# Kernel tuning notes

Measured on AMD Instinct MI355X. Metric: run time of the kernel, lower is better.

Reference implementation:

```python
import jax, jax.numpy as jnp
import numpy as np

D_MODEL = 1024
N_HEADS = 16
D_HEAD = D_MODEL // N_HEADS
D_FF = 4 * D_MODEL
B, T = 2, 2048
LN_EPS = 1e-5


def layer_norm(x, g, b):
    mu = jnp.mean(x, axis=-1, keepdims=True)
    var = jnp.mean(jnp.square(x - mu), axis=-1, keepdims=True)
    return (x - mu) * jax.lax.rsqrt(var + LN_EPS) * g + b


def setup_inputs() -> dict:
    key = jax.random.key(0)
    ks = jax.random.split(key, 8)
    s = lambda fan: 1.0 / np.sqrt(fan)
    return {
        "x": jax.random.normal(ks[0], (B, T, D_MODEL), dtype=jnp.float32),
        "ln1_g": jnp.ones((D_MODEL,), jnp.float32),
        "ln1_b": jnp.zeros((D_MODEL,), jnp.float32),
        "Wqkv": jax.random.normal(ks[1], (D_MODEL, 3 * D_MODEL), jnp.float32) * s(D_MODEL),
        "Wout": jax.random.normal(ks[2], (D_MODEL, D_MODEL), jnp.float32) * s(D_MODEL),
        "ln2_g": jnp.ones((D_MODEL,), jnp.float32),
        "ln2_b": jnp.zeros((D_MODEL,), jnp.float32),
        "W1": jax.random.normal(ks[3], (D_MODEL, D_FF), jnp.float32) * s(D_MODEL),
        "b1": jnp.zeros((D_FF,), jnp.float32),
        "W2": jax.random.normal(ks[4], (D_FF, D_MODEL), jnp.float32) * s(D_FF),
        "b2": jnp.zeros((D_MODEL,), jnp.float32),
    }


def attention(x, Wqkv, Wout):
    Bx, Tx, C = x.shape
    qkv = x @ Wqkv  # [B,T,3C]
    q, k, v = jnp.split(qkv, 3, axis=-1)
    q = q.reshape(Bx, Tx, N_HEADS, D_HEAD)
    k = k.reshape(Bx, Tx, N_HEADS, D_HEAD)
    v = v.reshape(Bx, Tx, N_HEADS, D_HEAD)
    scores = jnp.einsum('bqhd,bkhd->bhqk', q, k) / np.sqrt(D_HEAD).astype(np.float32)
    causal = jnp.tril(jnp.ones((Tx, Tx), dtype=bool))
    scores = jnp.where(causal, scores, -jnp.inf)
    attn = jax.nn.softmax(scores, axis=-1)
    out = jnp.einsum('bhqk,bkhd->bqhd', attn, v).reshape(Bx, Tx, C)
    return out @ Wout


def reference(x, ln1_g, ln1_b, Wqkv, Wout, ln2_g, ln2_b, W1, b1, W2, b2):
    x = x + attention(layer_norm(x, ln1_g, ln1_b), Wqkv, Wout)
    h = layer_norm(x, ln2_g, ln2_b)
    h = jax.nn.gelu(h @ W1 + b1, approximate=False) @ W2 + b2
    return x + h
```

## Files before the change

### kernel.cpp

```cpp
#include <hip/hip_runtime.h>
#include <math.h>

typedef __bf16 bf16;
typedef __bf16 bf16x4 __attribute__((ext_vector_type(4)));
typedef __bf16 bf16x8 __attribute__((ext_vector_type(8)));
typedef float  f32x4  __attribute__((ext_vector_type(4)));

#define MFMA16(a,b,c) __builtin_amdgcn_mfma_f32_16x16x32_bf16((a),(b),(c),0,0,0)

static __device__ __forceinline__ bf16x8 combine8(const bf16* plo, const bf16* phi) {
  bf16x4 lo = *(const bf16x4*)plo;
  bf16x4 hi = *(const bf16x4*)phi;
  return __builtin_shufflevector(lo, hi, 0, 1, 2, 3, 4, 5, 6, 7);
}

__global__ __launch_bounds__(256) void transpose_cast(const float* __restrict__ W,
                                                      bf16* __restrict__ WT,
                                                      int K, int N) {
  __shared__ float t[32][33];
  int n0 = blockIdx.x * 32, k0 = blockIdx.y * 32;
  int tx = threadIdx.x, ty = threadIdx.y;
#pragma unroll
  for (int i = 0; i < 32; i += 8)
    t[ty + i][tx] = W[(size_t)(k0 + ty + i) * N + n0 + tx];
  __syncthreads();
#pragma unroll
  for (int i = 0; i < 32; i += 8)
    WT[(size_t)(n0 + ty + i) * K + k0 + tx] = (bf16)t[tx][ty + i];
}

__global__ __launch_bounds__(256) void ln_kernel(const float* __restrict__ X,
                                                 const float* __restrict__ g,
                                                 const float* __restrict__ bta,
                                                 bf16* __restrict__ out) {
  int row  = blockIdx.x * 4 + (threadIdx.x >> 6);
  int lane = threadIdx.x & 63;
  const float4* x4 = (const float4*)(X + (size_t)row * 1024);
  float4 v[4];
  float s = 0.f, ss = 0.f;
#pragma unroll
  for (int i = 0; i < 4; ++i) {
    v[i] = x4[i * 64 + lane];
    s  += v[i].x + v[i].y + v[i].z + v[i].w;
    ss += v[i].x * v[i].x + v[i].y * v[i].y + v[i].z * v[i].z + v[i].w * v[i].w;
  }
#pragma unroll
  for (int off = 1; off < 64; off <<= 1) {
    s  += __shfl_xor(s, off, 64);
    ss += __shfl_xor(ss, off, 64);
  }
  float mu  = s * (1.0f / 1024.0f);
  float var = ss * (1.0f / 1024.0f) - mu * mu;
  float rs  = rsqrtf(var + 1e-5f);
  bf16* orow = out + (size_t)row * 1024;
#pragma unroll
  for (int i = 0; i < 4; ++i) {
    int c = i * 256 + lane * 4;
    bf16x4 pk;
    pk[0] = (bf16)((v[i].x - mu) * rs * g[c + 0] + bta[c + 0]);
    pk[1] = (bf16)((v[i].y - mu) * rs * g[c + 1] + bta[c + 1]);
    pk[2] = (bf16)((v[i].z - mu) * rs * g[c + 2] + bta[c + 2]);
    pk[3] = (bf16)((v[i].w - mu) * rs * g[c + 3] + bta[c + 3]);
    *(bf16x4*)(orow + c) = pk;
  }
}

template <int NR>
static __device__ __forceinline__ void stage2(const bf16* const* srcs, int koff,
                                              unsigned char* lds_base, int wv) {
#pragma unroll
  for (int i = 0; i < NR; ++i)
    __builtin_amdgcn_global_load_lds(
        (const __attribute__((address_space(1))) void*)(srcs[i] + koff),
        (__attribute__((address_space(3))) void*)(lds_base + (wv * (NR * 8) + i * 8) * 128),
        16, 0, 0);
}

static __device__ __forceinline__ bf16x8 frag_ld(const unsigned char* lds_base,
                                                 int r, int u) {
  return *(const bf16x8*)(lds_base + r * 128 + (((u ^ (r & 7)) & 7) << 4));
}

static __device__ __forceinline__ float gelu_tanh(float v) {
  float t = 0.7978845608028654f * (v + 0.044715f * v * v * v);
  t = fminf(t, 15.0f);
  float e = __builtin_amdgcn_exp2f(2.8853900817779268f * t);
  float th = (e - 1.0f) * __builtin_amdgcn_rcpf(e + 1.0f);
  return 0.5f * v * (1.0f + th);
}

template <int EPI, int BM>
__global__ __launch_bounds__(256) void gemm_bt(const bf16* __restrict__ A,
                                               const bf16* __restrict__ BT,
                                               int K, int N, int gx,
                                               const float* __restrict__ bias,
                                               const float* __restrict__ res,
                                               bf16* __restrict__ outb,
                                               float* __restrict__ outf) {
  constexpr int MI = BM / 32;
  constexpr int ANR = BM / 32;
  constexpr int TILE = (BM + 128) * 128;
  __shared__ unsigned char smem[TILE * 2];
  int nwg = gridDim.x, bid = blockIdx.x;
  int nb = (bid & 7) * (nwg >> 3) + (bid >> 3);
  int bx = nb % gx, by = nb / gx;
  int brow = by * BM, bcol = bx * 128;
  int tid = threadIdx.x, wv = tid >> 6, lane = tid & 63;
  int l15 = lane & 15, l4 = lane >> 4;
  int wm = wv >> 1, wn = wv & 1;
  f32x4 acc[MI][4] = {};

  int sr = lane >> 3;
  int su = (lane & 7) ^ sr;
  const bf16* aptr[ANR];
#pragma unroll
  for (int i = 0; i < ANR; ++i)
    aptr[i] = A + (size_t)(brow + wv * (ANR * 8) + i * 8 + sr) * K + su * 8;
  const bf16* bptr[4];
#pragma unroll
  for (int i = 0; i < 4; ++i)
    bptr[i] = BT + (size_t)(bcol + wv * 32 + i * 8 + sr) * K + su * 8;

  stage2<ANR>(aptr, 0, smem, wv);
  stage2<4>(bptr, 0, smem + BM * 128, wv);
  __syncthreads();
  int cur = 0;
  for (int k0 = 0; k0 < K; k0 += 64) {
    unsigned char* sc = smem + cur * TILE;
    if (k0 + 64 < K) {
      unsigned char* sn = smem + (cur ^ 1) * TILE;
      stage2<ANR>(aptr, k0 + 64, sn, wv);
      stage2<4>(bptr, k0 + 64, sn + BM * 128, wv);
    }
    unsigned char* As = sc;
    unsigned char* Bs = sc + BM * 128;
#pragma unroll
    for (int ks = 0; ks < 2; ++ks) {
      bf16x8 af[MI], bfr[4];
#pragma unroll
      for (int mi = 0; mi < MI; ++mi)
        af[mi] = frag_ld(As, wm * (BM / 2) + mi * 16 + l15, ks * 4 + l4);
#pragma unroll
      for (int ni = 0; ni < 4; ++ni)
        bfr[ni] = frag_ld(Bs, wn * 64 + ni * 16 + l15, ks * 4 + l4);
#pragma unroll
      for (int mi = 0; mi < MI; ++mi)
#pragma unroll
        for (int ni = 0; ni < 4; ++ni)
          acc[mi][ni] = MFMA16(af[mi], bfr[ni], acc[mi][ni]);
    }
    __syncthreads();
    cur ^= 1;
  }
#pragma unroll
  for (int mi = 0; mi < MI; ++mi) {
#pragma unroll
    for (int ni = 0; ni < 4; ++ni) {
      int col  = bcol + wn * 64 + ni * 16 + l15;
      int row0 = brow + wm * (BM / 2) + mi * 16 + l4 * 4;
#pragma unroll
      for (int r = 0; r < 4; ++r) {
        int row = row0 + r;
        float v = acc[mi][ni][r];
        if (EPI == 1) {
          v += bias[col];
          v = gelu_tanh(v);
        }
        if (EPI == 2) v += res[(size_t)row * N + col];
        if (EPI == 3) v += bias[col] + res[(size_t)row * N + col];
        if (EPI == 0 || EPI == 1) outb[(size_t)row * N + col] = (bf16)v;
        else                      outf[(size_t)row * N + col] = v;
      }
    }
  }
}

__global__ __launch_bounds__(256) void pack_kv(const bf16* __restrict__ qkv,
                                               bf16* __restrict__ kpack,
                                               bf16* __restrict__ vpack) {
  int blk = blockIdx.x;
  int wv = threadIdx.x >> 6, lane = threadIdx.x & 63;
  int l15 = lane & 15, l4 = lane >> 4;
  int ch = (blk & 15) * 4 + wv;
  int bh = blk >> 4;
  int b = bh >> 4, h = bh & 15;
  const bf16* kq = qkv + (size_t)b * 2048 * 3072 + 1024 + h * 64;
  const bf16* vq = kq + 1024;
#pragma unroll
  for (int fr = 0; fr < 4; ++fr) {
    int key = ch * 32 + ((fr >> 1) << 4) + l15;
    int dbase = ((fr & 1) << 5) + l4 * 4;
    bf16x8 v = combine8(kq + (size_t)key * 3072 + dbase,
                        kq + (size_t)key * 3072 + dbase + 16);
    *(bf16x8*)(kpack + ((size_t)(bh * 64 + ch) * 4 + fr) * 512 + lane * 8) = v;
  }
#pragma unroll
  for (int db = 0; db < 4; ++db) {
    int d = db * 16 + l15;
    bf16x8 v;
#pragma unroll
    for (int j = 0; j < 8; ++j) {
      int key = ch * 32 + l4 * 4 + (j & 3) + ((j >> 2) << 4);
      v[j] = vq[(size_t)key * 3072 + d];
    }
    *(bf16x8*)(vpack + ((size_t)(bh * 64 + ch) * 4 + db) * 512 + lane * 8) = v;
  }
}

static __device__ __forceinline__ void proc_chunk(
    const bf16x8* __restrict__ kf, const bf16x8* __restrict__ vf,
    const bf16x8 (* __restrict__ qf)[2], f32x4 (* __restrict__ o)[4],
    float* __restrict__ lsum, bool diag, int l15, int l4) {
  const float SC = 0.125f * 1.4426950408889634f;
#pragma unroll
  for (int f = 0; f < 2; ++f) {
    f32x4 c0 = {0.f, 0.f, 0.f, 0.f}, c1 = {0.f, 0.f, 0.f, 0.f};
    c0 = MFMA16(kf[0], qf[f][0], c0);
    c0 = MFMA16(kf[1], qf[f][1], c0);
    c1 = MFMA16(kf[2], qf[f][0], c1);
    c1 = MFMA16(kf[3], qf[f][1], c1);
    bf16x8 pf;
    float ls = 0.f;
#pragma unroll
    for (int r = 0; r < 4; ++r) {
      float e0 = __builtin_amdgcn_exp2f(c0[r] * SC);
      float e1 = __builtin_amdgcn_exp2f(c1[r] * SC);
      if (diag) {
        int qg = f * 16 + l15;
        int key = l4 * 4 + r;
        if (key > qg)      e0 = 0.f;
        if (key + 16 > qg) e1 = 0.f;
      }
      ls += e0 + e1;
      pf[r]     = (bf16)e0;
      pf[4 + r] = (bf16)e1;
    }
    lsum[f] += ls;
    o[f][0] = MFMA16(vf[0], pf, o[f][0]);
    o[f][1] = MFMA16(vf[1], pf, o[f][1]);
    o[f][2] = MFMA16(vf[2], pf, o[f][2]);
    o[f][3] = MFMA16(vf[3], pf, o[f][3]);
  }
}

__global__ __launch_bounds__(256) void attn_kernel(const bf16* __restrict__ qkv,
                                                   const bf16* __restrict__ kpack,
                                                   const bf16* __restrict__ vpack,
                                                   bf16* __restrict__ attn_out) {
  __shared__ float mbuf[3 * 68 * 64];
  int bid = blockIdx.x;
  int nb = (bid & 7) * 128 + (bid >> 3);
  int bh = nb >> 5, j = nb & 31;
  int b = bh >> 4, h = bh & 15;
  int wv = threadIdx.x >> 6, lane = threadIdx.x & 63;
  int l15 = lane & 15, l4 = lane >> 4;
  int qc[2] = {j, 63 - j};
  const bf16* base = qkv + (size_t)b * 2048 * 3072;
  int d0 = l4 * 4;
  bf16x8 qf[2][2][2];
#pragma unroll
  for (int c = 0; c < 2; ++c)
#pragma unroll
    for (int f = 0; f < 2; ++f) {
      const bf16* qp = base + (size_t)(qc[c] * 32 + f * 16 + l15) * 3072 + h * 64;
      qf[c][f][0] = combine8(qp + d0,      qp + d0 + 16);
      qf[c][f][1] = combine8(qp + d0 + 32, qp + d0 + 48);
    }
  const bf16* kp0 = kpack + (size_t)bh * 64 * 2048 + lane * 8;
  const bf16* vp0 = vpack + (size_t)bh * 64 * 2048 + lane * 8;

  f32x4 o[2][2][4] = {};
  float lsum[2][2] = {};

  for (int ch = wv; ch <= qc[1]; ch += 4) {
    const bf16* kp = kp0 + (size_t)ch * 2048;
    const bf16* vp = vp0 + (size_t)ch * 2048;
    bf16x8 kf[4], vf[4];
    kf[0] = *(const bf16x8*)(kp);
    kf[1] = *(const bf16x8*)(kp + 512);
    kf[2] = *(const bf16x8*)(kp + 1024);
    kf[3] = *(const bf16x8*)(kp + 1536);
    vf[0] = *(const bf16x8*)(vp);
    vf[1] = *(const bf16x8*)(vp + 512);
    vf[2] = *(const bf16x8*)(vp + 1024);
    vf[3] = *(const bf16x8*)(vp + 1536);
    if (ch <= qc[0])
      proc_chunk(kf, vf, qf[0], o[0], lsum[0], ch == qc[0], l15, l4);
    proc_chunk(kf, vf, qf[1], o[1], lsum[1], ch == qc[1], l15, l4);
  }

  if (wv > 0) {
    float* dst = mbuf + (wv - 1) * 68 * 64 + lane;
#pragma unroll
    for (int c = 0; c < 2; ++c)
#pragma unroll
      for (int f = 0; f < 2; ++f) {
#pragma unroll
        for (int db = 0; db < 4; ++db)
#pragma unroll
          for (int r = 0; r < 4; ++r)
            dst[(c * 32 + f * 16 + db * 4 + r) * 64] = o[c][f][db][r];
        dst[(64 + c * 2 + f) * 64] = lsum[c][f];
      }
  }
  __syncthreads();
  if (wv == 0) {
#pragma unroll
    for (int w = 0; w < 3; ++w) {
      const float* src = mbuf + w * 68 * 64 + lane;
#pragma unroll
      for (int c = 0; c < 2; ++c)
#pragma unroll
        for (int f = 0; f < 2; ++f) {
#pragma unroll
          for (int db = 0; db < 4; ++db)
#pragma unroll
            for (int r = 0; r < 4; ++r)
              o[c][f][db][r] += src[(c * 32 + f * 16 + db * 4 + r) * 64];
          lsum[c][f] += src[(64 + c * 2 + f) * 64];
        }
    }
#pragma unroll
    for (int c = 0; c < 2; ++c)
#pragma unroll
      for (int f = 0; f < 2; ++f) {
        float l = lsum[c][f];
        l += __shfl_xor(l, 16, 64);
        l += __shfl_xor(l, 32, 64);
        float inv = 1.0f / l;
#pragma unroll
        for (int db = 0; db < 4; ++db)
#pragma unroll
          for (int r = 0; r < 4; ++r) {
            int d = db * 16 + l4 * 4 + r;
            attn_out[(size_t)(b * 2048 + qc[c] * 32 + f * 16 + l15) * 1024 +
                     h * 64 + d] = (bf16)(o[c][f][db][r] * inv);
          }
      }
  }
}

extern "C" void kernel_launch(void* const* d_in, const int* in_sizes, int n_in,
                              void* d_out, int out_size, void* d_ws, size_t ws_size,
                              hipStream_t stream) {
  const float* x     = (const float*)d_in[0];
  const float* ln1g  = (const float*)d_in[1];
  const float* ln1b  = (const float*)d_in[2];
  const float* Wqkv  = (const float*)d_in[3];
  const float* Wout  = (const float*)d_in[4];
  const float* ln2g  = (const float*)d_in[5];
  const float* ln2b  = (const float*)d_in[6];
  const float* W1    = (const float*)d_in[7];
  const float* b1    = (const float*)d_in[8];
  const float* W2    = (const float*)d_in[9];
  const float* b2    = (const float*)d_in[10];
  float* out = (float*)d_out;

  char* p = (char*)d_ws;
  bf16* WqkvT = (bf16*)p; p += (size_t)3072 * 1024 * 2;
  bf16* WoutT = (bf16*)p; p += (size_t)1024 * 1024 * 2;
  bf16* W1T   = (bf16*)p; p += (size_t)4096 * 1024 * 2;
  bf16* W2T   = (bf16*)p; p += (size_t)1024 * 4096 * 2;
  bf16* hbuf  = (bf16*)p; p += (size_t)4096 * 1024 * 2;
  bf16* aobuf = (bf16*)p; p += (size_t)4096 * 1024 * 2;
  bf16* big   = (bf16*)p; p += (size_t)4096 * 4096 * 2;

  bf16* kpack = big + (size_t)4096 * 3072;
  bf16* vpack = hbuf;

  dim3 tb(32, 8);
  transpose_cast<<<dim3(96, 32),  tb, 0, stream>>>(Wqkv, WqkvT, 1024, 3072);
  transpose_cast<<<dim3(32, 32),  tb, 0, stream>>>(Wout, WoutT, 1024, 1024);
  transpose_cast<<<dim3(128, 32), tb, 0, stream>>>(W1,   W1T,   1024, 4096);
  transpose_cast<<<dim3(32, 128), tb, 0, stream>>>(W2,   W2T,   4096, 1024);

  ln_kernel<<<1024, 256, 0, stream>>>(x, ln1g, ln1b, hbuf);
  gemm_bt<0, 128><<<768, 256, 0, stream>>>(hbuf, WqkvT, 1024, 3072, 24,
                                           nullptr, nullptr, big, nullptr);
  pack_kv<<<512, 256, 0, stream>>>(big, kpack, vpack);
  attn_kernel<<<1024, 256, 0, stream>>>(big, kpack, vpack, aobuf);
  gemm_bt<2, 64><<<512, 256, 0, stream>>>(aobuf, WoutT, 1024, 1024, 8,
                                          nullptr, x, nullptr, out);
  ln_kernel<<<1024, 256, 0, stream>>>(out, ln2g, ln2b, hbuf);
  gemm_bt<1, 128><<<1024, 256, 0, stream>>>(hbuf, W1T, 1024, 4096, 32,
                                            b1, nullptr, big, nullptr);
  gemm_bt<3, 64><<<512, 256, 0, stream>>>(big, W2T, 4096, 1024, 8,
                                          b2, out, nullptr, out);
}
```

Before: 217.1 us.

## Triple-buffer GEMM LDS stages with explicit vmcnt waits

Moves the GEMM main loop from double to triple buffering in LDS, issuing loads two K-tiles ahead. Instead of a full __syncthreads, it waits only until the oldest tile's global-to-LDS loads have completed (partial vmcnt), then barriers. This hides more global memory latency behind MFMA work. In exchange it uses more shared memory, which may lower occupancy, and it relies on stage2 issuing exactly NLD vector loads per tile, so the hand-coded waitcnt values must match.

After: 241.1 us. +11.0%, slower.

```diff
diff --git a/kernel.cpp b/kernel.cpp
--- a/kernel.cpp
+++ b/kernel.cpp
@@ -12,6 +12,13 @@
   bf16x4 lo = *(const bf16x4*)plo;
   bf16x4 hi = *(const bf16x4*)phi;
   return __builtin_shufflevector(lo, hi, 0, 1, 2, 3, 4, 5, 6, 7);
+}
+
+template <int N>
+static __device__ __forceinline__ void wait_vm() {
+  if constexpr (N == 0)      asm volatile("s_waitcnt vmcnt(0)" ::: "memory");
+  else if constexpr (N == 6) asm volatile("s_waitcnt vmcnt(6)" ::: "memory");
+  else if constexpr (N == 8) asm volatile("s_waitcnt vmcnt(8)" ::: "memory");
 }
 
 __global__ __launch_bounds__(256) void transpose_cast(const float* __restrict__ W,
@@ -99,8 +106,9 @@
                                                float* __restrict__ outf) {
   constexpr int MI = BM / 32;
   constexpr int ANR = BM / 32;
+  constexpr int NLD = ANR + 4;
   constexpr int TILE = (BM + 128) * 128;
-  __shared__ unsigned char smem[TILE * 2];
+  __shared__ unsigned char smem[TILE * 3];
   int nwg = gridDim.x, bid = blockIdx.x;
   int nb = (bid & 7) * (nwg >> 3) + (bid >> 3);
   int bx = nb % gx, by = nb / gx;
@@ -121,16 +129,23 @@
   for (int i = 0; i < 4; ++i)
     bptr[i] = BT + (size_t)(bcol + wv * 32 + i * 8 + sr) * K + su * 8;
 
+  const int nt = K >> 6;
   stage2<ANR>(aptr, 0, smem, wv);
   stage2<4>(bptr, 0, smem + BM * 128, wv);
-  __syncthreads();
+  stage2<ANR>(aptr, 64, smem + TILE, wv);
+  stage2<4>(bptr, 64, smem + TILE + BM * 128, wv);
+  wait_vm<NLD>();
+  __builtin_amdgcn_s_barrier();
+  __builtin_amdgcn_sched_barrier(0);
+
   int cur = 0;
-  for (int k0 = 0; k0 < K; k0 += 64) {
+  for (int t = 0; t < nt; ++t) {
     unsigned char* sc = smem + cur * TILE;
-    if (k0 + 64 < K) {
-      unsigned char* sn = smem + (cur ^ 1) * TILE;
-      stage2<ANR>(aptr, k0 + 64, sn, wv);
-      stage2<4>(bptr, k0 + 64, sn + BM * 128, wv);
+    if (t + 2 < nt) {
+      int nn = cur + 2; if (nn >= 3) nn -= 3;
+      unsigned char* sn = smem + nn * TILE;
+      stage2<ANR>(aptr, (t + 2) * 64, sn, wv);
+      stage2<4>(bptr, (t + 2) * 64, sn + BM * 128, wv);
     }
     unsigned char* As = sc;
     unsigned char* Bs = sc + BM * 128;
@@ -149,8 +164,13 @@
         for (int ni = 0; ni < 4; ++ni)
           acc[mi][ni] = MFMA16(af[mi], bfr[ni], acc[mi][ni]);
     }
-    __syncthreads();
-    cur ^= 1;
+    if (t + 1 < nt) {
+      if (t + 2 < nt) wait_vm<NLD>();
+      else            wait_vm<0>();
+      __builtin_amdgcn_s_barrier();
+      __builtin_amdgcn_sched_barrier(0);
+    }
+    if (++cur == 3) cur = 0;
   }
 #pragma unroll
   for (int mi = 0; mi < MI; ++mi) {
```
